# Optimization experiments

Measured on AMD Instinct MI355X. Metric: run time of the kernel, lower is better.

Reference implementation:

```python
import jax, jax.numpy as jnp
import numpy as np

B, L = 32, 512
D_EMB = 500      # tagger_mlp_layer
LANG = 100       # tagger_embeddings_size
H = 800          # tagger_encoder_size * 2
P_ARC = 100      # parser_arc_proj_size
P_LAB = 400      # parser_label_proj_size
MLP = 500        # tagger_mlp_layer (aux_mlp out)
N_LANG, N_LAB, N_UPOS, N_XPOS, N_ATTRS = 8, 50, 20, 300, 500


def setup_inputs() -> dict:
    key = jax.random.key(0)
    ks = jax.random.split(key, 24)
    s = 0.05
    lang_table = jax.random.normal(ks[3], (N_LANG, LANG), jnp.float32) * s
    lang_table = lang_table.at[0].set(0.0)  # padding_idx=0
    return {
        "emb": jax.random.normal(ks[0], (B, L, D_EMB), jnp.float32),
        "hidden": jax.random.normal(ks[1], (B, L, H), jnp.float32),
        "lang_ids": jax.random.randint(ks[2], (B,), 0, N_LANG),
        "lang_table": lang_table,
        "W_arc": jax.random.normal(ks[4], (P_ARC, D_EMB + LANG), jnp.float32) * s,
        "b_arc": jax.random.normal(ks[5], (P_ARC,), jnp.float32) * s,
        "W_lab": jax.random.normal(ks[6], (P_LAB, D_EMB + LANG), jnp.float32) * s,
        "b_lab": jax.random.normal(ks[7], (P_LAB,), jnp.float32) * s,
        "w_head": jax.random.normal(ks[8], (2 * P_ARC,), jnp.float32) * s,
        "b_head": jax.random.normal(ks[9], (1,), jnp.float32) * s,
        "W_aux": jax.random.normal(ks[10], (MLP, H), jnp.float32) * s,
        "b_aux": jax.random.normal(ks[11], (MLP,), jnp.float32) * s,
        "W_upos": jax.random.normal(ks[12], (N_UPOS, MLP + LANG), jnp.float32) * s,
        "b_upos": jax.random.normal(ks[13], (N_UPOS,), jnp.float32) * s,
        "W_xpos": jax.random.normal(ks[14], (N_XPOS, MLP + LANG), jnp.float32) * s,
        "b_xpos": jax.random.normal(ks[15], (N_XPOS,), jnp.float32) * s,
        "W_attrs": jax.random.normal(ks[16], (N_ATTRS, MLP + LANG), jnp.float32) * s,
        "b_attrs": jax.random.normal(ks[17], (N_ATTRS,), jnp.float32) * s,
    }


def reference(emb, hidden, lang_ids, lang_table, W_arc, b_arc, W_lab, b_lab,
              w_head, b_head, W_aux, b_aux, W_upos, b_upos, W_xpos, b_xpos,
              W_attrs, b_attrs):
    Bv, Lv = emb.shape[0], emb.shape[1]
    lang_emb = lang_table[lang_ids]                              # [B, LANG]
    lang_rep = jnp.broadcast_to(lang_emb[:, None, :], (Bv, Lv, lang_emb.shape[-1]))
    ho = jnp.concatenate((emb, lang_rep), axis=2)                # [B, L, D_EMB+LANG]

    proj_arc = jnp.tanh(jnp.einsum('bld,pd->blp', ho, W_arc) + b_arc)   # [B, L, P_ARC]
    proj_label = jnp.tanh(jnp.einsum('bld,pd->blp', ho, W_lab) + b_lab) # [B, L, P_LAB]

    # Biaffine decomposition of output_head(cat(pa[i], pa[j])):
    # score(i,j) = pa[i] . w1 + pa[j] . w2 + b
    P = proj_arc.shape[-1]
    s1 = proj_arc @ w_head[:P]                                   # [B, L]
    s2 = proj_arc @ w_head[P:]                                   # [B, L]
    core = s1[:, :, None] + s2[:, None, :] + b_head[0]           # [B, L, L]
    arcs = jnp.concatenate(
        (jnp.zeros((Bv, Lv, 1), core.dtype), core), axis=2)     # [B, L, L+1]

    aux_hid = jnp.tanh(jnp.einsum('blh,mh->blm', hidden, W_aux) + b_aux)  # [B, L, MLP]
    aux_cat = jnp.concatenate((aux_hid, lang_rep), axis=2)
    s_upos = jnp.einsum('blm,um->blu', aux_cat, W_upos) + b_upos
    s_xpos = jnp.einsum('blm,um->blu', aux_cat, W_xpos) + b_xpos
    s_attrs = jnp.einsum('blm,um->blu', aux_cat, W_attrs) + b_attrs
    return arcs, proj_label, s_upos, s_xpos, s_attrs
```

## Files before the change

kernel.cpp:

```cpp
#include <hip/hip_runtime.h>


using f16   = _Float16;
using f16x4 = __attribute__((ext_vector_type(4))) _Float16;
using f16x8 = __attribute__((ext_vector_type(8))) _Float16;
using f32x4 = __attribute__((ext_vector_type(4))) float;

#define M_ROWS 16384

__device__ __forceinline__ f16 f2h(float f) { return (f16)f; }
__device__ __forceinline__ f16x4 cvt4(float4 v) {
  return f16x4{ f2h(v.x), f2h(v.y), f2h(v.z), f2h(v.w) };
}

__device__ __forceinline__ void async16(void* lds, const void* gp) {
  __builtin_amdgcn_global_load_lds(
      (const __attribute__((address_space(1))) unsigned int*)gp,
      (__attribute__((address_space(3))) unsigned int*)lds, 16, 0, 0);
}

__global__ __launch_bounds__(256) void setup_kernel(
    const float* __restrict__ emb, const float* __restrict__ hidden,
    const float* __restrict__ lang_table, const int* __restrict__ lang_ids,
    const float* __restrict__ W_arc, const float* __restrict__ b_arc,
    const float* __restrict__ W_lab, const float* __restrict__ b_lab,
    const float* __restrict__ W_aux, const float* __restrict__ b_aux,
    const float* __restrict__ W_upos, const float* __restrict__ b_upos,
    const float* __restrict__ W_xpos, const float* __restrict__ b_xpos,
    const float* __restrict__ W_attrs, const float* __restrict__ b_attrs,
    f16* __restrict__ ho, f16* __restrict__ aux_cat, f16* __restrict__ hid16,
    f16* __restrict__ W_proj, f16* __restrict__ W_auxp, f16* __restrict__ W_heads,
    float* __restrict__ bias_proj, float* __restrict__ bias_aux, float* __restrict__ bias_heads)
{
  const int HID_Q = 3276800;
  const int HO_Q  = 2621440;
  const int W_Q   = 327680;
  const int TOTAL = HID_Q + HO_Q + W_Q;

  for (int q = blockIdx.x * 256 + threadIdx.x; q < TOTAL; q += gridDim.x * 256) {
    if (q < HID_Q) {
      float4 v = *(const float4*)(hidden + 4 * (size_t)q);
      *(f16x4*)(hid16 + 4 * (size_t)q) = cvt4(v);
    } else if (q < HID_Q + HO_Q) {
      int p = q - HID_Q;
      int row = p / 160;
      int s = p - row * 160;
      f16* horow = ho + (size_t)row * 640;
      if (s < 125) {
        float4 v = *(const float4*)(emb + (size_t)row * 500 + 4 * s);
        *(f16x4*)(horow + 4 * s) = cvt4(v);
      } else {
        f16x4 h = { (f16)0.f, (f16)0.f, (f16)0.f, (f16)0.f };
        if (s < 150) {
          const float* lrow = lang_table + (size_t)lang_ids[row >> 9] * 100;
          float4 v = *(const float4*)(lrow + (s - 125) * 4);
          h = cvt4(v);
        }
        *(f16x4*)(horow + 4 * s) = h;
        *(f16x4*)(aux_cat + (size_t)row * 640 + 4 * s) = h;
      }
    } else {
      int w = q - (HID_Q + HO_Q);
      const float* src = nullptr;
      f16* dst;
      if (w < 81920) {
        int n = w / 160, s = w - n * 160;
        dst = W_proj + (size_t)w * 4;
        if (s < 150 && n < 500)
          src = (n < 100 ? W_arc + (size_t)n * 600
                         : W_lab + (size_t)(n - 100) * 600) + s * 4;
      } else if (w < 184320) {
        int w2 = w - 81920;
        int n = w2 / 200;
        dst = W_auxp + (size_t)w2 * 4;
        if (n < 500) src = W_aux + (size_t)w2 * 4;
      } else {
        int w3 = w - 184320;
        int n = w3 / 160, s = w3 - n * 160;
        dst = W_heads + (size_t)w3 * 4;
        if (s < 150 && n < 820)
          src = (n < 20 ? W_upos + (size_t)n * 600
                : n < 320 ? W_xpos + (size_t)(n - 20) * 600
                          : W_attrs + (size_t)(n - 320) * 600) + s * 4;
      }
      f16x4 h = { (f16)0.f, (f16)0.f, (f16)0.f, (f16)0.f };
      if (src) h = cvt4(*(const float4*)src);
      *(f16x4*)dst = h;
    }
  }

  if (blockIdx.x == 0) {
    for (int idx = threadIdx.x; idx < 1920; idx += 256) {
      if (idx < 512) {
        float v = 0.f;
        if (idx < 100)      v = b_arc[idx];
        else if (idx < 500) v = b_lab[idx - 100];
        bias_proj[idx] = v;
      } else if (idx < 1024) {
        int i = idx - 512;
        bias_aux[i] = (i < 500) ? b_aux[i] : 0.f;
      } else {
        int i = idx - 1024; float v = 0.f;
        if (i < 20)       v = b_upos[i];
        else if (i < 320) v = b_xpos[i - 20];
        else if (i < 820) v = b_attrs[i - 320];
        bias_heads[i] = v;
      }
    }
  }
}

__device__ __forceinline__ void gemm_core(
    const f16* __restrict__ A, const f16* __restrict__ B, const int K,
    const int bm, const int bn,
    f16 (*ldsA)[128 * 32], f16 (*ldsB)[128 * 32], f32x4 (&acc)[4][4])
{
  const int tid  = threadIdx.x;
  const int lane = tid & 63;
  const int wave = tid >> 6;
  const int wm = wave >> 1, wn = wave & 1;
  const int m16 = lane & 15, quad = lane >> 4;

  const int q0 = tid, q1 = tid + 256;
  const f16* gA0 = A + (size_t)(bm * 128 + (q0 >> 2)) * K + (q0 & 3) * 8;
  const f16* gA1 = A + (size_t)(bm * 128 + (q1 >> 2)) * K + (q1 & 3) * 8;
  const f16* gB0 = B + (size_t)(bn * 128 + (q0 >> 2)) * K + (q0 & 3) * 8;
  const f16* gB1 = B + (size_t)(bn * 128 + (q1 >> 2)) * K + (q1 & 3) * 8;

#define STAGE(buf, k0) do {                                        \
    async16(&((uint4*)ldsA[buf])[wave * 64],       gA0 + (k0));    \
    async16(&((uint4*)ldsA[buf])[wave * 64 + 256], gA1 + (k0));    \
    async16(&((uint4*)ldsB[buf])[wave * 64],       gB0 + (k0));    \
    async16(&((uint4*)ldsB[buf])[wave * 64 + 256], gB1 + (k0));    \
  } while (0)

#define COMPUTE(buf) do {                                                        \
    f16x8 af[4], bfr[4];                                                         \
    _Pragma("unroll")                                                            \
    for (int i = 0; i < 4; ++i)                                                  \
      af[i] = *(const f16x8*)&ldsA[buf][(wm * 64 + i * 16 + m16) * 32 + quad * 8]; \
    _Pragma("unroll")                                                            \
    for (int j = 0; j < 4; ++j)                                                  \
      bfr[j] = *(const f16x8*)&ldsB[buf][(wn * 64 + j * 16 + m16) * 32 + quad * 8]; \
    _Pragma("unroll")                                                            \
    for (int i = 0; i < 4; ++i)                                                  \
      _Pragma("unroll")                                                          \
      for (int j = 0; j < 4; ++j)                                                \
        acc[i][j] = __builtin_amdgcn_mfma_f32_16x16x32_f16(af[i], bfr[j], acc[i][j], 0, 0, 0); \
  } while (0)

  STAGE(0, 0);
  __syncthreads();
  int cur = 0;
  for (int k0 = 32; k0 < K; k0 += 32) {
    STAGE(cur ^ 1, k0);
    COMPUTE(cur);
    __syncthreads();
    cur ^= 1;
  }
  COMPUTE(cur);
#undef STAGE
#undef COMPUTE
}

__global__ __launch_bounds__(256) void gemm01(
    const f16* __restrict__ ho, const f16* __restrict__ hid16,
    const f16* __restrict__ W_proj, const f16* __restrict__ W_auxp,
    const float* __restrict__ bias_proj, const float* __restrict__ bias_aux,
    float* __restrict__ out_label, const float* __restrict__ w_head,
    float* __restrict__ s1, float* __restrict__ s2, f16* __restrict__ aux_cat)
{
  __shared__ __align__(16) f16 ldsA[2][128 * 32];
  __shared__ __align__(16) f16 ldsB[2][128 * 32];
  __shared__ float s1red[2][128], s2red[2][128];

  const int tid  = threadIdx.x;
  const int lane = tid & 63;
  const int wave = tid >> 6;
  const int wm = wave >> 1, wn = wave & 1;
  const int m16 = lane & 15, quad = lane >> 4;
  const int bm  = blockIdx.x;
  const int bny = blockIdx.y;
  const bool is0 = (bny < 4);
  const int bn  = is0 ? bny : bny - 4;

  const f16* A = is0 ? ho : hid16;
  const f16* B = is0 ? W_proj : W_auxp;
  const float* bias = is0 ? bias_proj : bias_aux;
  const int K = is0 ? 640 : 800;

  f32x4 acc[4][4] = {};
  gemm_core(A, B, K, bm, bn, ldsA, ldsB, acc);

  const int row0 = bm * 128 + wm * 64 + quad * 4;
  const int col0 = bn * 128 + wn * 64 + m16;

  if (is0) {
    float p1[4][4] = {}, p2[4][4] = {};
    const bool isbn0 = (bn == 0);
#pragma unroll
    for (int i = 0; i < 4; ++i) {
#pragma unroll
      for (int j = 0; j < 4; ++j) {
        const int col = col0 + j * 16;
        const float bcol = bias[col];
        float w1c = 0.f, w2c = 0.f;
        if (isbn0 && col < 100) { w1c = w_head[col]; w2c = w_head[100 + col]; }
#pragma unroll
        for (int r = 0; r < 4; ++r) {
          const int row = row0 + i * 16 + r;
          float v = tanhf(acc[i][j][r] + bcol);
          if (col >= 100 && col < 500) out_label[(size_t)row * 400 + col - 100] = v;
          p1[i][r] += v * w1c;
          p2[i][r] += v * w2c;
        }
      }
    }
    if (isbn0) {
#pragma unroll
      for (int d = 1; d < 16; d <<= 1) {
#pragma unroll
        for (int i = 0; i < 4; ++i)
#pragma unroll
          for (int r = 0; r < 4; ++r) {
            p1[i][r] += __shfl_xor(p1[i][r], d);
            p2[i][r] += __shfl_xor(p2[i][r], d);
          }
      }
      if (m16 == 0) {
#pragma unroll
        for (int i = 0; i < 4; ++i)
#pragma unroll
          for (int r = 0; r < 4; ++r) {
            int rl = wm * 64 + i * 16 + quad * 4 + r;
            s1red[wn][rl] = p1[i][r];
            s2red[wn][rl] = p2[i][r];
          }
      }
      __syncthreads();
      if (tid < 128)       s1[bm * 128 + tid] = s1red[0][tid] + s1red[1][tid];
      else                 s2[bm * 128 + tid - 128] = s2red[0][tid - 128] + s2red[1][tid - 128];
    }
  } else {
#pragma unroll
    for (int i = 0; i < 4; ++i)
#pragma unroll
      for (int j = 0; j < 4; ++j) {
        const int col = col0 + j * 16;
        const float bcol = bias[col];
#pragma unroll
        for (int r = 0; r < 4; ++r) {
          const int row = row0 + i * 16 + r;
          if (col < 500) aux_cat[(size_t)row * 640 + col] = f2h(tanhf(acc[i][j][r] + bcol));
        }
      }
  }
}

__global__ __launch_bounds__(256) void gemm2_arcs(
    const f16* __restrict__ aux_cat, const f16* __restrict__ W_heads,
    const float* __restrict__ bias_heads,
    const float* __restrict__ s1, const float* __restrict__ s2,
    const float* __restrict__ b_head,
    float* __restrict__ out_arcs, float* __restrict__ out_upos,
    float* __restrict__ out_xpos, float* __restrict__ out_attrs)
{
  __shared__ __align__(16) f16 ldsA[2][128 * 32];
  __shared__ __align__(16) f16 ldsB[2][128 * 32];
  __shared__ float s2s[512];

  const int bm = blockIdx.x, bn = blockIdx.y;

  if (bn == 7) {
    const int r0 = bm * 128;
    const int b = r0 >> 9;
    const float bh = b_head[0];
    for (int j = threadIdx.x; j < 512; j += 256) s2s[j] = s2[(b << 9) + j];
    __syncthreads();
    for (int rr = 0; rr < 128; ++rr) {
      const int row = r0 + rr;
      const float s1v = s1[row] + bh;
      float* orow = out_arcs + (size_t)row * 513;
      if (threadIdx.x == 0) orow[0] = 0.f;
#pragma unroll
      for (int j = threadIdx.x; j < 512; j += 256)
        orow[1 + j] = s1v + s2s[j];
    }
    return;
  }

  const int tid  = threadIdx.x;
  const int lane = tid & 63;
  const int wave = tid >> 6;
  const int wm = wave >> 1, wn = wave & 1;
  const int m16 = lane & 15, quad = lane >> 4;

  f32x4 acc[4][4] = {};
  gemm_core(aux_cat, W_heads, 640, bm, bn, ldsA, ldsB, acc);

  const int row0 = bm * 128 + wm * 64 + quad * 4;
  const int col0 = bn * 128 + wn * 64 + m16;
#pragma unroll
  for (int i = 0; i < 4; ++i)
#pragma unroll
    for (int j = 0; j < 4; ++j) {
      const int col = col0 + j * 16;
      const float bcol = bias_heads[col];
#pragma unroll
      for (int r = 0; r < 4; ++r) {
        const int row = row0 + i * 16 + r;
        float v = acc[i][j][r] + bcol;
        if (col < 20)        out_upos[(size_t)row * 20 + col] = v;
        else if (col < 320)  out_xpos[(size_t)row * 300 + col - 20] = v;
        else if (col < 820)  out_attrs[(size_t)row * 500 + col - 320] = v;
      }
    }
}

extern "C" void kernel_launch(void* const* d_in, const int* in_sizes, int n_in,
                              void* d_out, int out_size, void* d_ws, size_t ws_size,
                              hipStream_t stream)
{
  const float* emb      = (const float*)d_in[0];
  const float* hidden   = (const float*)d_in[1];
  const int*   lang_ids = (const int*)d_in[2];
  const float* lang_tab = (const float*)d_in[3];
  const float* W_arc  = (const float*)d_in[4];
  const float* b_arc  = (const float*)d_in[5];
  const float* W_lab  = (const float*)d_in[6];
  const float* b_lab  = (const float*)d_in[7];
  const float* w_head = (const float*)d_in[8];
  const float* b_head = (const float*)d_in[9];
  const float* W_aux  = (const float*)d_in[10];
  const float* b_aux  = (const float*)d_in[11];
  const float* W_upos = (const float*)d_in[12];
  const float* b_upos = (const float*)d_in[13];
  const float* W_xpos = (const float*)d_in[14];
  const float* b_xpos = (const float*)d_in[15];
  const float* W_attrs = (const float*)d_in[16];
  const float* b_attrs = (const float*)d_in[17];

  char* ws = (char*)d_ws;
  f16* ho      = (f16*)(ws + 0);
  f16* aux_cat = (f16*)(ws + 20971520);
  f16* hid16   = (f16*)(ws + 41943040);
  f16* W_proj  = (f16*)(ws + 68157440);
  f16* W_auxp  = (f16*)(ws + 68812800);
  f16* W_heads = (f16*)(ws + 69632000);
  float* bias_proj  = (float*)(ws + 70778880);
  float* bias_aux   = (float*)(ws + 70780928);
  float* bias_heads = (float*)(ws + 70782976);
  float* s1         = (float*)(ws + 70786560);
  float* s2         = (float*)(ws + 70852096);

  float* out       = (float*)d_out;
  float* out_arcs  = out;
  float* out_label = out + 8404992;
  float* out_upos  = out + 14958592;
  float* out_xpos  = out + 15286272;
  float* out_attrs = out + 20201472;

  setup_kernel<<<2048, 256, 0, stream>>>(
      emb, hidden, lang_tab, lang_ids,
      W_arc, b_arc, W_lab, b_lab, W_aux, b_aux,
      W_upos, b_upos, W_xpos, b_xpos, W_attrs, b_attrs,
      ho, aux_cat, hid16, W_proj, W_auxp, W_heads,
      bias_proj, bias_aux, bias_heads);

  gemm01<<<dim3(128, 8), 256, 0, stream>>>(
      ho, hid16, W_proj, W_auxp, bias_proj, bias_aux,
      out_label, w_head, s1, s2, aux_cat);

  gemm2_arcs<<<dim3(128, 8), 256, 0, stream>>>(
      aux_cat, W_heads, bias_heads, s1, s2, b_head,
      out_arcs, out_upos, out_xpos, out_attrs);
}
```

Before: 331.3 us.

## Triple-buffer GEMM K-loop with vmcnt waits and use fast exp-based tanh

Replaces the double-buffered LDS K-loop with a three-stage pipeline that issues loads two tiles ahead. It waits on vmcnt counters plus a raw s_barrier instead of a full __syncthreads each iteration, so global loads overlap with MFMA compute. It also swaps tanhf for an exp2/rcp approximation to cut epilogue cost. The cost is 50% more LDS per block, which may lower occupancy, and slightly lower tanh accuracy.

New measurement: 322.2 us. 1.03x faster.

```diff
diff --git a/kernel.cpp b/kernel.cpp
--- a/kernel.cpp
+++ b/kernel.cpp
@@ -11,6 +11,12 @@
 __device__ __forceinline__ f16 f2h(float f) { return (f16)f; }
 __device__ __forceinline__ f16x4 cvt4(float4 v) {
   return f16x4{ f2h(v.x), f2h(v.y), f2h(v.z), f2h(v.w) };
+}
+
+__device__ __forceinline__ float fast_tanh(float x) {
+  float xc = fminf(fmaxf(x, -15.f), 15.f);
+  float e  = __builtin_amdgcn_exp2f(xc * 2.885390081777927f);
+  return 1.f - 2.f * __builtin_amdgcn_rcpf(e + 1.f);
 }
 
 __device__ __forceinline__ void async16(void* lds, const void* gp) {
@@ -149,16 +155,25 @@
         acc[i][j] = __builtin_amdgcn_mfma_f32_16x16x32_f16(af[i], bfr[j], acc[i][j], 0, 0, 0); \
   } while (0)
 
+  const int NT = K >> 5;
   STAGE(0, 0);
-  __syncthreads();
-  int cur = 0;
-  for (int k0 = 32; k0 < K; k0 += 32) {
-    STAGE(cur ^ 1, k0);
-    COMPUTE(cur);
-    __syncthreads();
-    cur ^= 1;
-  }
-  COMPUTE(cur);
+  STAGE(1, 32);
+  asm volatile("s_waitcnt vmcnt(4)" ::: "memory");
+  __builtin_amdgcn_s_barrier();
+  __builtin_amdgcn_sched_barrier(0);
+
+  int c0 = 0, c1 = 1, c2 = 2;
+  for (int t = 0; t < NT; ++t) {
+    if (t + 2 < NT) STAGE(c2, (t + 2) << 5);
+    COMPUTE(c0);
+    if (t + 1 < NT) {
+      if (t + 2 < NT) asm volatile("s_waitcnt vmcnt(4)" ::: "memory");
+      else            asm volatile("s_waitcnt vmcnt(0)" ::: "memory");
+      __builtin_amdgcn_s_barrier();
+      __builtin_amdgcn_sched_barrier(0);
+      int tmp = c0; c0 = c1; c1 = c2; c2 = tmp;
+    }
+  }
 #undef STAGE
 #undef COMPUTE
 }
@@ -170,8 +185,8 @@
     float* __restrict__ out_label, const float* __restrict__ w_head,
     float* __restrict__ s1, float* __restrict__ s2, f16* __restrict__ aux_cat)
 {
-  __shared__ __align__(16) f16 ldsA[2][128 * 32];
-  __shared__ __align__(16) f16 ldsB[2][128 * 32];
+  __shared__ __align__(16) f16 ldsA[3][128 * 32];
+  __shared__ __align__(16) f16 ldsB[3][128 * 32];
   __shared__ float s1red[2][128], s2red[2][128];
 
   const int tid  = threadIdx.x;
@@ -209,7 +224,7 @@
 #pragma unroll
         for (int r = 0; r < 4; ++r) {
           const int row = row0 + i * 16 + r;
-          float v = tanhf(acc[i][j][r] + bcol);
+          float v = fast_tanh(acc[i][j][r] + bcol);
           if (col >= 100 && col < 500) out_label[(size_t)row * 400 + col - 100] = v;
           p1[i][r] += v * w1c;
           p2[i][r] += v * w2c;
@@ -251,7 +266,7 @@
 #pragma unroll
         for (int r = 0; r < 4; ++r) {
           const int row = row0 + i * 16 + r;
-          if (col < 500) aux_cat[(size_t)row * 640 + col] = f2h(tanhf(acc[i][j][r] + bcol));
+          if (col < 500) aux_cat[(size_t)row * 640 + col] = f2h(fast_tanh(acc[i][j][r] + bcol));
         }
       }
   }
@@ -265,8 +280,8 @@
     float* __restrict__ out_arcs, float* __restrict__ out_upos,
     float* __restrict__ out_xpos, float* __restrict__ out_attrs)
 {
-  __shared__ __align__(16) f16 ldsA[2][128 * 32];
-  __shared__ __align__(16) f16 ldsB[2][128 * 32];
+  __shared__ __align__(16) f16 ldsA[3][128 * 32];
+  __shared__ __align__(16) f16 ldsB[3][128 * 32];
   __shared__ float s2s[512];
 
   const int bm = blockIdx.x, bn = blockIdx.y;
```
